# Performance work log

Measured on AMD Instinct MI355X. Metric: run time of the kernel, lower is better.

The kernel has to match this reference:

```python
import jax, jax.numpy as jnp
import numpy as np

B, S, D, H, L = 4, 2048, 512, 8, 128
HD = D // H  # head dim = 64


def setup_inputs() -> dict:
    key = jax.random.key(0)
    ks = jax.random.split(key, 20)
    sc = 0.05
    return {
        "query": jax.random.normal(ks[0], (B, S, D), jnp.float32),
        "key": jax.random.normal(ks[1], (B, S, D), jnp.float32),
        "value": jax.random.normal(ks[2], (B, S, D), jnp.float32),
        "Wq": jax.random.normal(ks[3], (D, D), jnp.float32) * sc,
        "bq": jax.random.normal(ks[4], (D,), jnp.float32) * sc,
        "Wk": jax.random.normal(ks[5], (D, D), jnp.float32) * sc,
        "bk": jax.random.normal(ks[6], (D,), jnp.float32) * sc,
        "Wv": jax.random.normal(ks[7], (D, D), jnp.float32) * sc,
        "bv": jax.random.normal(ks[8], (D,), jnp.float32) * sc,
        "Wo": jax.random.normal(ks[9], (D, D), jnp.float32) * sc,
        "bo": jax.random.normal(ks[10], (D,), jnp.float32) * sc,
        "Wg": jax.random.normal(ks[11], (D, L), jnp.float32) * sc,
        "bg": jax.random.normal(ks[12], (L,), jnp.float32) * sc,
        "Wmq": jax.random.normal(ks[13], (L, D), jnp.float32) * sc,
        "bmq": jax.random.normal(ks[14], (D,), jnp.float32) * sc,
        "Wmk": jax.random.normal(ks[15], (L, D), jnp.float32) * sc,
        "bmk": jax.random.normal(ks[16], (D,), jnp.float32) * sc,
    }


def reference(query, key, value, Wq, bq, Wk, bk, Wv, bv, Wo, bo, Wg, bg, Wmq, bmq, Wmk, bmk):
    # latent-gated modulation of Q and K (computed from query)
    latent = jax.nn.relu(query @ Wg + bg)                 # [B,S,L]
    mod_q = jax.nn.sigmoid(latent @ Wmq + bmq)            # [B,S,D]
    mod_k = jax.nn.sigmoid(latent @ Wmk + bmk)            # [B,S,D]
    q = (query @ Wq + bq) * mod_q
    k = (key @ Wk + bk) * mod_k
    v = value @ Wv + bv
    # split heads: [B,S,D] -> [B,S,H,HD]
    q = q.reshape(B, S, H, HD)
    k = k.reshape(B, S, H, HD)
    v = v.reshape(B, S, H, HD)
    scale = 1.0 / jnp.sqrt(jnp.float32(HD))
    scores = jnp.einsum("bqhd,bkhd->bhqk", q, k) * scale  # [B,H,S,S]
    attn_weights = jax.nn.softmax(scores, axis=-1)
    attn_out = jnp.einsum("bhqk,bkhd->bqhd", attn_weights, v).reshape(B, S, D)
    output = attn_out @ Wo + bo
    return output, attn_weights
```

## Files before the change

### kernel.cpp

```cpp
#include <hip/hip_runtime.h>
#include <hip/hip_bf16.h>

#define BB 4
#define SS 2048
#define DD 512
#define HH 8
#define HDIM 64

typedef __attribute__((ext_vector_type(8))) short bf16x8;
typedef __attribute__((ext_vector_type(4))) float floatx4;
typedef __attribute__((ext_vector_type(8))) unsigned short u16x8;

static __device__ __forceinline__ unsigned short f2bf(float x) {
  __hip_bfloat16 h = __float2bfloat16(x);
  unsigned short u;
  __builtin_memcpy(&u, &h, sizeof(u));
  return u;
}
static __device__ __forceinline__ float bf2f(unsigned short u) {
  union { unsigned int i; float f; } c;
  c.i = ((unsigned int)u) << 16;
  return c.f;
}
static __device__ __forceinline__ void split1(float x, unsigned short& h, unsigned short& l) {
  h = f2bf(x);
  l = f2bf(x - bf2f(h));
}
static __device__ __forceinline__ void gload_lds16(const void* g, void* l) {
  __builtin_amdgcn_global_load_lds((const __attribute__((address_space(1))) void*)g,
                                   (__attribute__((address_space(3))) void*)l, 16, 0, 0);
}

#define SWZ(row, col) ((col) ^ (((row) & 7) * 8))

static __device__ __forceinline__ void stage_tile(unsigned short* dst,
    const unsigned short* src, size_t rstride, int wid, int lane) {
#pragma unroll
  for (int it = 0; it < 2; ++it) {
    const int base = it * 256 + wid * 64;
    const int c = base + lane;
    const int row = c >> 3, uu = c & 7;
    gload_lds16(src + (size_t)row * rstride + ((uu ^ (row & 7)) * 8),
                dst + (size_t)base * 8);
  }
}

__global__ __launch_bounds__(256)
void wsplit_kernel(const float* __restrict__ Wq, const float* __restrict__ Wk,
                   const float* __restrict__ Wv, const float* __restrict__ Wo,
                   const float* __restrict__ Wg, const float* __restrict__ Wmq,
                   const float* __restrict__ Wmk, unsigned short* __restrict__ wsb)
{
  const int bx = blockIdx.x;
  const float* src; unsigned short* dh; unsigned short* dl; int K, N, tile;
  if (bx < 64)       { src = Wq;  dh = wsb + 0;       dl = wsb + 262144;  K = 512; N = 512; tile = bx; }
  else if (bx < 128) { src = Wk;  dh = wsb + 524288;  dl = wsb + 786432;  K = 512; N = 512; tile = bx - 64; }
  else if (bx < 192) { src = Wv;  dh = wsb + 1048576; dl = wsb + 1310720; K = 512; N = 512; tile = bx - 128; }
  else if (bx < 256) { src = Wo;  dh = wsb + 1572864; dl = wsb + 1835008; K = 512; N = 512; tile = bx - 192; }
  else if (bx < 272) { src = Wg;  dh = wsb + 2097152; dl = wsb + 2162688; K = 512; N = 128; tile = bx - 256; }
  else if (bx < 288) { src = Wmq; dh = wsb + 2228224; dl = wsb + 2293760; K = 128; N = 512; tile = bx - 272; }
  else               { src = Wmk; dh = wsb + 2359296; dl = wsb + 2424832; K = 128; N = 512; tile = bx - 288; }
  const int nt = N >> 6;
  const int k0 = (tile / nt) * 64, n0 = (tile % nt) * 64;
  __shared__ float T[64][65];
  const int t = threadIdx.x;
  const int r = t >> 2, c = (t & 3) * 16;
#pragma unroll
  for (int j = 0; j < 16; j += 4)
    *(float4*)&T[r][c + j] = *(const float4*)&src[(size_t)(k0 + r) * N + n0 + c + j];
  __syncthreads();
  u16x8 hv[2], lv[2];
#pragma unroll
  for (int j = 0; j < 16; ++j) {
    unsigned short h, l;
    split1(T[c + j][r], h, l);
    hv[j >> 3][j & 7] = h;
    lv[j >> 3][j & 7] = l;
  }
  const size_t di = (size_t)(n0 + r) * K + k0 + c;
  *(u16x8*)&dh[di]     = hv[0];
  *(u16x8*)&dh[di + 8] = hv[1];
  *(u16x8*)&dl[di]     = lv[0];
  *(u16x8*)&dl[di + 8] = lv[1];
}

template<int BM, int BN>
static __device__ __forceinline__ void gemm_phase(
    const float* __restrict__ A, const unsigned short* __restrict__ WHp,
    const unsigned short* __restrict__ WLp, const int K,
    const int m0, const int n0,
    unsigned short (*Ah)[32], unsigned short (*Al)[32],
    unsigned short (*Bh)[32], unsigned short (*Bl)[32],
    floatx4 (*acc)[BN / 32])
{
  constexpr int HM = BM / 2, HN = BN / 2, FM = BM / 32, FN = BN / 32;
  constexpr int TPR = 256 / BM;
  constexpr int CPT = 32 / TPR;
  constexpr int WCH = BN / 16;
  constexpr int WPW = (2 * WCH) / 4;
  const int t = threadIdx.x;
  const int wid = t >> 6, lane = t & 63, quad = lane >> 4, l16 = lane & 15;
  const int wm = wid >> 1, wn = wid & 1;
  const int arow = t / TPR, acol = (t % TPR) * CPT;
  const int asw = (arow & 3) * 8;

  for (int k0 = 0; k0 < K; k0 += 32) {
    __syncthreads();
#pragma unroll
    for (int cc = 0; cc < WPW; ++cc) {
      const int cid = wid * WPW + cc;
      const int pl = cid / WCH, ch = cid - pl * WCH;
      const int row = ch * 16 + (lane >> 2);
      const int kof = ((lane & 3) ^ ((lane >> 2) & 3)) * 8;
      const unsigned short* g = (pl ? WLp : WHp) + (size_t)(n0 + row) * K + k0 + kof;
      gload_lds16(g, (pl ? Bl : Bh)[ch * 16]);
    }
    {
      const float* ga = A + (size_t)(m0 + arow) * K + k0 + acol;
#pragma unroll
      for (int j = 0; j < CPT; j += 4) {
        float4 f = *(const float4*)(ga + j);
        unsigned short h[4], l[4];
        split1(f.x, h[0], l[0]); split1(f.y, h[1], l[1]);
        split1(f.z, h[2], l[2]); split1(f.w, h[3], l[3]);
        *(ushort4*)&Ah[arow][(acol + j) ^ asw] = make_ushort4(h[0], h[1], h[2], h[3]);
        *(ushort4*)&Al[arow][(acol + j) ^ asw] = make_ushort4(l[0], l[1], l[2], l[3]);
      }
    }
    __syncthreads();
    const int swf = (l16 & 3) * 8;
    bf16x8 fah[FM], fal[FM], fbh[FN], fbl[FN];
#pragma unroll
    for (int mi = 0; mi < FM; ++mi) {
      const int rr = wm * HM + mi * 16 + l16;
      fah[mi] = *(const bf16x8*)&Ah[rr][(quad * 8) ^ swf];
      fal[mi] = *(const bf16x8*)&Al[rr][(quad * 8) ^ swf];
    }
#pragma unroll
    for (int ni = 0; ni < FN; ++ni) {
      const int rr = wn * HN + ni * 16 + l16;
      fbh[ni] = *(const bf16x8*)&Bh[rr][(quad * 8) ^ swf];
      fbl[ni] = *(const bf16x8*)&Bl[rr][(quad * 8) ^ swf];
    }
#pragma unroll
    for (int mi = 0; mi < FM; ++mi)
#pragma unroll
      for (int ni = 0; ni < FN; ++ni) {
        acc[mi][ni] = __builtin_amdgcn_mfma_f32_16x16x32_bf16(fah[mi], fbh[ni], acc[mi][ni], 0, 0, 0);
        acc[mi][ni] = __builtin_amdgcn_mfma_f32_16x16x32_bf16(fal[mi], fbh[ni], acc[mi][ni], 0, 0, 0);
        acc[mi][ni] = __builtin_amdgcn_mfma_f32_16x16x32_bf16(fah[mi], fbl[ni], acc[mi][ni], 0, 0, 0);
      }
  }
}

template<int BM, int BN, int EPI>
__global__ __launch_bounds__(256, 2)
void mgemm_kernel(const float* __restrict__ A, const unsigned short* __restrict__ WH,
                  const unsigned short* __restrict__ WL, const float* __restrict__ bias,
                  const float* __restrict__ modf, const float sc,
                  float* __restrict__ Cf, unsigned short* __restrict__ C16,
                  int K, int N)
{
  constexpr int HM = BM / 2, HN = BN / 2, FM = BM / 32, FN = BN / 32;
  __shared__ alignas(16) unsigned short Ah[BM][32], Al[BM][32], Bh[BN][32], Bl[BN][32];
  const int t = threadIdx.x;
  const int wid = t >> 6, lane = t & 63, quad = lane >> 4, l16 = lane & 15;
  const int wm = wid >> 1, wn = wid & 1;
  const int m0 = blockIdx.y * BM, n0 = blockIdx.x * BN;

  floatx4 acc[FM][FN];
#pragma unroll
  for (int i = 0; i < FM; ++i)
#pragma unroll
    for (int j = 0; j < FN; ++j) {
      floatx4 z = {0.f, 0.f, 0.f, 0.f};
      acc[i][j] = z;
    }

  gemm_phase<BM, BN>(A, WH, WL, K, m0, n0, Ah, Al, Bh, Bl, acc);

#pragma unroll
  for (int ni = 0; ni < FN; ++ni) {
    const int col = n0 + wn * HN + ni * 16 + l16;
    const float b1 = bias[col];
#pragma unroll
    for (int mi = 0; mi < FM; ++mi)
#pragma unroll
      for (int r = 0; r < 4; ++r) {
        const int row = m0 + wm * HM + mi * 16 + quad * 4 + r;
        float v = acc[mi][ni][r] + b1;
        if constexpr (EPI == 0) {
          Cf[(size_t)row * N + col] = v;
        } else if constexpr (EPI == 1) {
          Cf[(size_t)row * N + col] = fmaxf(v, 0.f);
        } else if constexpr (EPI == 2) {
          C16[(size_t)row * N + col] = f2bf(v);
        } else if constexpr (EPI == 4) {
          const float m = modf[(size_t)row * N + col];
          C16[(size_t)row * N + col] = f2bf(v * m * sc);
        } else {
          Cf[(size_t)row * N + col] = 1.f / (1.f + __expf(-v));
        }
      }
  }
}

__global__ __launch_bounds__(256)
void vtrans_kernel(const unsigned short* __restrict__ V16, unsigned short* __restrict__ Vt)
{
  __shared__ unsigned short T[64][72];
  const int x  = blockIdx.x;
  const int st = x & 31;
  const int h  = (x >> 5) & 7;
  const int b  = x >> 8;
  const int t  = threadIdx.x;
  const unsigned short* src = V16 + ((size_t)b * SS + st * 64) * DD + h * HDIM;
  for (int i = t; i < 1024; i += 256) {
    int r = i >> 4, c4 = (i & 15) * 4;
    *(ushort4*)&T[r][c4] = *(const ushort4*)&src[(size_t)r * DD + c4];
  }
  __syncthreads();
  unsigned short* dst = Vt + ((size_t)(b * HH + h) * HDIM) * SS + st * 64;
  for (int i = t; i < 1024; i += 256) {
    int hd = i >> 4, s4 = (i & 15) * 4;
    ushort4 u = make_ushort4(T[s4 + 0][hd], T[s4 + 1][hd], T[s4 + 2][hd], T[s4 + 3][hd]);
    *(ushort4*)&dst[(size_t)hd * SS + s4] = u;
  }
}

__global__ __launch_bounds__(256, 3)
void attn_kernel(const unsigned short* __restrict__ Q16,
                 const unsigned short* __restrict__ K16,
                 const unsigned short* __restrict__ Vt,
                 float* __restrict__ AW, float* __restrict__ AO)
{
  __shared__ alignas(16) unsigned short Qs[64][64];
  __shared__ alignas(16) unsigned short Ks[2][64][64];
  __shared__ alignas(16) unsigned short Vs[2][64][64];
  __shared__ alignas(16) unsigned short Ps[4][16][64];

  const int t    = threadIdx.x;
  const int wid  = t >> 6;
  const int lane = t & 63;
  const int quad = lane >> 4;
  const int l16  = lane & 15;
  const int x  = blockIdx.x;
  const int j  = x >> 3;
  const int g  = ((j >> 5) << 3) | (x & 7);
  const int qb = j & 31;
  const int b  = g >> 3;
  const int h  = g & 7;
  const int q0 = qb * 64;

  const unsigned short* Qg = Q16 + ((size_t)b * SS + q0) * DD + h * HDIM;
  const unsigned short* Kg = K16 + (size_t)b * SS * DD + h * HDIM;
  const unsigned short* Vg = Vt + ((size_t)(b * HH + h) * HDIM) * SS;

  stage_tile(&Qs[0][0], Qg, DD, wid, lane);
  stage_tile(&Ks[0][0][0], Kg, DD, wid, lane);
  __syncthreads();

  const bf16x8 a0 = *(const bf16x8*)&Qs[wid * 16 + l16][SWZ(l16, quad * 8)];
  const bf16x8 a1 = *(const bf16x8*)&Qs[wid * 16 + l16][SWZ(l16, 32 + quad * 8)];

  float lsum[4] = {0.f, 0.f, 0.f, 0.f};
  for (int kt = 0; kt < SS / 64; ++kt) {
    const int cur = kt & 1;
    if (kt < 31)
      stage_tile(&Ks[cur ^ 1][0][0], Kg + (size_t)(kt + 1) * 64 * DD, DD, wid, lane);
#pragma unroll
    for (int kst = 0; kst < 4; ++kst) {
      bf16x8 bb0 = *(const bf16x8*)&Ks[cur][kst * 16 + l16][SWZ(l16, quad * 8)];
      bf16x8 bb1 = *(const bf16x8*)&Ks[cur][kst * 16 + l16][SWZ(l16, 32 + quad * 8)];
      floatx4 cc = {0.f, 0.f, 0.f, 0.f};
      cc = __builtin_amdgcn_mfma_f32_16x16x32_bf16(a0, bb0, cc, 0, 0, 0);
      cc = __builtin_amdgcn_mfma_f32_16x16x32_bf16(a1, bb1, cc, 0, 0, 0);
#pragma unroll
      for (int r = 0; r < 4; ++r) lsum[r] += __expf(cc[r]);
    }
    __syncthreads();
  }
#pragma unroll
  for (int r = 0; r < 4; ++r) {
    float v = lsum[r];
    v += __shfl_xor(v, 1, 64); v += __shfl_xor(v, 2, 64);
    v += __shfl_xor(v, 4, 64); v += __shfl_xor(v, 8, 64);
    lsum[r] = 1.f / v;
  }

  floatx4 o[4];
#pragma unroll
  for (int n = 0; n < 4; ++n) { floatx4 z = {0.f, 0.f, 0.f, 0.f}; o[n] = z; }

  const size_t awb = ((size_t)(b * HH + h) * SS + q0 + wid * 16) * SS;

  stage_tile(&Ks[0][0][0], Kg, DD, wid, lane);
  stage_tile(&Vs[0][0][0], Vg, SS, wid, lane);
  __syncthreads();
  for (int kt = 0; kt < SS / 64; ++kt) {
    const int cur = kt & 1;
    if (kt < 31) {
      stage_tile(&Ks[cur ^ 1][0][0], Kg + (size_t)(kt + 1) * 64 * DD, DD, wid, lane);
      stage_tile(&Vs[cur ^ 1][0][0], Vg + (size_t)(kt + 1) * 64, SS, wid, lane);
    }
#pragma unroll
    for (int kst = 0; kst < 4; ++kst) {
      bf16x8 bb0 = *(const bf16x8*)&Ks[cur][kst * 16 + l16][SWZ(l16, quad * 8)];
      bf16x8 bb1 = *(const bf16x8*)&Ks[cur][kst * 16 + l16][SWZ(l16, 32 + quad * 8)];
      floatx4 cc = {0.f, 0.f, 0.f, 0.f};
      cc = __builtin_amdgcn_mfma_f32_16x16x32_bf16(a0, bb0, cc, 0, 0, 0);
      cc = __builtin_amdgcn_mfma_f32_16x16x32_bf16(a1, bb1, cc, 0, 0, 0);
#pragma unroll
      for (int r = 0; r < 4; ++r) {
        const float wv = __expf(cc[r]) * lsum[r];
        AW[awb + (size_t)(quad * 4 + r) * SS + kt * 64 + kst * 16 + l16] = wv;
        Ps[wid][quad * 4 + r][SWZ(quad * 4 + r, kst * 16 + l16)] = f2bf(wv);
      }
    }
#pragma unroll
    for (int c2 = 0; c2 < 2; ++c2) {
      bf16x8 ap = *(const bf16x8*)&Ps[wid][l16][SWZ(l16, c2 * 32 + quad * 8)];
#pragma unroll
      for (int n = 0; n < 4; ++n) {
        bf16x8 bv = *(const bf16x8*)&Vs[cur][n * 16 + l16][SWZ(l16, c2 * 32 + quad * 8)];
        o[n] = __builtin_amdgcn_mfma_f32_16x16x32_bf16(ap, bv, o[n], 0, 0, 0);
      }
    }
    __syncthreads();
  }
  float* AOg = AO + ((size_t)b * SS + q0 + wid * 16) * DD + h * HDIM;
#pragma unroll
  for (int n = 0; n < 4; ++n)
#pragma unroll
    for (int r = 0; r < 4; ++r)
      AOg[(size_t)(quad * 4 + r) * DD + n * 16 + l16] = o[n][r];
}

extern "C" void kernel_launch(void* const* d_in, const int* in_sizes, int n_in,
                              void* d_out, int out_size, void* d_ws, size_t ws_size,
                              hipStream_t stream) {
  (void)in_sizes; (void)n_in; (void)out_size; (void)ws_size;
  const float* query = (const float*)d_in[0];
  const float* key_i = (const float*)d_in[1];
  const float* value = (const float*)d_in[2];
  const float* Wq  = (const float*)d_in[3];
  const float* bq  = (const float*)d_in[4];
  const float* Wk  = (const float*)d_in[5];
  const float* bk  = (const float*)d_in[6];
  const float* Wv  = (const float*)d_in[7];
  const float* bv  = (const float*)d_in[8];
  const float* Wo  = (const float*)d_in[9];
  const float* bo  = (const float*)d_in[10];
  const float* Wg  = (const float*)d_in[11];
  const float* bg  = (const float*)d_in[12];
  const float* Wmq = (const float*)d_in[13];
  const float* bmq = (const float*)d_in[14];
  const float* Wmk = (const float*)d_in[15];
  const float* bmk = (const float*)d_in[16];

  float* out = (float*)d_out;
  float* AW  = out + (size_t)BB * SS * DD;

  char* ws = (char*)d_ws;
  unsigned short* ws16 = (unsigned short*)ws;
  unsigned short* q16 = (unsigned short*)(ws + (5u  << 20));
  unsigned short* k16 = (unsigned short*)(ws + (13u << 20));
  unsigned short* vt  = (unsigned short*)(ws + (21u << 20));
  float*          lat = (float*)(ws + (29u << 20));
  float*          X   = (float*)(ws + (33u << 20));
  unsigned short* v16 = (unsigned short*)(ws + (33u << 20));
  float*          ao  = (float*)(ws + (33u << 20));

  const size_t W_WQH = 0,       W_WQL = 262144;
  const size_t W_WKH = 524288,  W_WKL = 786432;
  const size_t W_WVH = 1048576, W_WVL = 1310720;
  const size_t W_WOH = 1572864, W_WOL = 1835008;
  const size_t W_WGH = 2097152, W_WGL = 2162688;
  const size_t W_WMQH = 2228224, W_WMQL = 2293760;
  const size_t W_WMKH = 2359296, W_WMKL = 2424832;

  dim3 blk(256);
  wsplit_kernel<<<dim3(304), blk, 0, stream>>>(Wq, Wk, Wv, Wo, Wg, Wmq, Wmk, ws16);
  mgemm_kernel<64, 64, 1><<<dim3(2, 128), blk, 0, stream>>>(
      query, ws16 + W_WGH, ws16 + W_WGL, bg, nullptr, 1.f, lat, nullptr, 512, 128);
  mgemm_kernel<64, 64, 5><<<dim3(8, 128), blk, 0, stream>>>(
      lat, ws16 + W_WMQH, ws16 + W_WMQL, bmq, nullptr, 1.f, X, nullptr, 128, 512);
  mgemm_kernel<128, 64, 4><<<dim3(8, 64), blk, 0, stream>>>(
      query, ws16 + W_WQH, ws16 + W_WQL, bq, X, 0.125f, nullptr, q16, 512, 512);
  mgemm_kernel<64, 64, 5><<<dim3(8, 128), blk, 0, stream>>>(
      lat, ws16 + W_WMKH, ws16 + W_WMKL, bmk, nullptr, 1.f, X, nullptr, 128, 512);
  mgemm_kernel<128, 64, 4><<<dim3(8, 64), blk, 0, stream>>>(
      key_i, ws16 + W_WKH, ws16 + W_WKL, bk, X, 1.f, nullptr, k16, 512, 512);
  mgemm_kernel<128, 64, 2><<<dim3(8, 64), blk, 0, stream>>>(
      value, ws16 + W_WVH, ws16 + W_WVL, bv, nullptr, 1.f, nullptr, v16, 512, 512);
  vtrans_kernel<<<dim3(1024), blk, 0, stream>>>(v16, vt);
  attn_kernel<<<dim3(1024), blk, 0, stream>>>(q16, k16, vt, AW, ao);
  mgemm_kernel<128, 64, 0><<<dim3(8, 64), blk, 0, stream>>>(
      ao, ws16 + W_WOH, ws16 + W_WOL, bo, nullptr, 1.f, out, nullptr, 512, 512);
}
```

Before: 865.9 us.

## Split attention row-sum pass into separate split-K kernel with 4x more blocks

The first pass that computes softmax denominators moves out of the attention kernel into its own kernel. That kernel splits the key dimension into four chunks across 4096 blocks and writes partial sums to workspace. The P·V kernel then reads and adds the four partials, and its Q fragments now load straight from global memory instead of through shared memory. The aim is more parallelism in the denominator pass and lower per-block latency in the main kernel. The cost is an extra launch, a partial-sum buffer, and dropping the occupancy hint of 3 blocks per SM.

```diff
diff --git a/kernel.cpp b/kernel.cpp
--- a/kernel.cpp
+++ b/kernel.cpp
@@ -228,45 +228,36 @@
   }
 }
 
-__global__ __launch_bounds__(256, 3)
-void attn_kernel(const unsigned short* __restrict__ Q16,
-                 const unsigned short* __restrict__ K16,
-                 const unsigned short* __restrict__ Vt,
-                 float* __restrict__ AW, float* __restrict__ AO)
-{
-  __shared__ alignas(16) unsigned short Qs[64][64];
+__global__ __launch_bounds__(256)
+void attn_lsum_kernel(const unsigned short* __restrict__ Q16,
+                      const unsigned short* __restrict__ K16,
+                      float* __restrict__ lsum4)
+{
   __shared__ alignas(16) unsigned short Ks[2][64][64];
-  __shared__ alignas(16) unsigned short Vs[2][64][64];
-  __shared__ alignas(16) unsigned short Ps[4][16][64];
-
-  const int t    = threadIdx.x;
-  const int wid  = t >> 6;
-  const int lane = t & 63;
-  const int quad = lane >> 4;
-  const int l16  = lane & 15;
-  const int x  = blockIdx.x;
-  const int j  = x >> 3;
-  const int g  = ((j >> 5) << 3) | (x & 7);
+  const int t = threadIdx.x, wid = t >> 6, lane = t & 63;
+  const int quad = lane >> 4, l16 = lane & 15;
+  const int x = blockIdx.x;
+  const int c = x >> 10;
+  const int y = x & 1023;
+  const int j = y >> 3;
+  const int g = ((j >> 5) << 3) | (y & 7);
   const int qb = j & 31;
-  const int b  = g >> 3;
-  const int h  = g & 7;
+  const int b = g >> 3, h = g & 7;
   const int q0 = qb * 64;
 
   const unsigned short* Qg = Q16 + ((size_t)b * SS + q0) * DD + h * HDIM;
-  const unsigned short* Kg = K16 + (size_t)b * SS * DD + h * HDIM;
-  const unsigned short* Vg = Vt + ((size_t)(b * HH + h) * HDIM) * SS;
-
-  stage_tile(&Qs[0][0], Qg, DD, wid, lane);
+  const unsigned short* Kg = K16 + (size_t)b * SS * DD + h * HDIM + (size_t)c * 512 * DD;
+
+  const bf16x8 a0 = *(const bf16x8*)&Qg[(size_t)(wid * 16 + l16) * DD + quad * 8];
+  const bf16x8 a1 = *(const bf16x8*)&Qg[(size_t)(wid * 16 + l16) * DD + 32 + quad * 8];
+
   stage_tile(&Ks[0][0][0], Kg, DD, wid, lane);
   __syncthreads();
 
-  const bf16x8 a0 = *(const bf16x8*)&Qs[wid * 16 + l16][SWZ(l16, quad * 8)];
-  const bf16x8 a1 = *(const bf16x8*)&Qs[wid * 16 + l16][SWZ(l16, 32 + quad * 8)];
-
   float lsum[4] = {0.f, 0.f, 0.f, 0.f};
-  for (int kt = 0; kt < SS / 64; ++kt) {
+  for (int kt = 0; kt < 8; ++kt) {
     const int cur = kt & 1;
-    if (kt < 31)
+    if (kt < 7)
       stage_tile(&Ks[cur ^ 1][0][0], Kg + (size_t)(kt + 1) * 64 * DD, DD, wid, lane);
 #pragma unroll
     for (int kst = 0; kst < 4; ++kst) {
@@ -285,18 +276,55 @@
     float v = lsum[r];
     v += __shfl_xor(v, 1, 64); v += __shfl_xor(v, 2, 64);
     v += __shfl_xor(v, 4, 64); v += __shfl_xor(v, 8, 64);
-    lsum[r] = 1.f / v;
-  }
-
-  floatx4 o[4];
-#pragma unroll
-  for (int n = 0; n < 4; ++n) { floatx4 z = {0.f, 0.f, 0.f, 0.f}; o[n] = z; }
-
-  const size_t awb = ((size_t)(b * HH + h) * SS + q0 + wid * 16) * SS;
+    if (l16 == 0)
+      lsum4[((size_t)g * SS + q0 + wid * 16 + quad * 4 + r) * 4 + c] = v;
+  }
+}
+
+__global__ __launch_bounds__(256)
+void attn_pv_kernel(const unsigned short* __restrict__ Q16,
+                    const unsigned short* __restrict__ K16,
+                    const unsigned short* __restrict__ Vt,
+                    const float* __restrict__ lsum4,
+                    float* __restrict__ AW, float* __restrict__ AO)
+{
+  __shared__ alignas(16) unsigned short Ks[2][64][64];
+  __shared__ alignas(16) unsigned short Vs[2][64][64];
+  __shared__ alignas(16) unsigned short Ps[4][16][64];
+
+  const int t = threadIdx.x, wid = t >> 6, lane = t & 63;
+  const int quad = lane >> 4, l16 = lane & 15;
+  const int x = blockIdx.x;
+  const int j = x >> 3;
+  const int g = ((j >> 5) << 3) | (x & 7);
+  const int qb = j & 31;
+  const int b = g >> 3, h = g & 7;
+  const int q0 = qb * 64;
+
+  const unsigned short* Qg = Q16 + ((size_t)b * SS + q0) * DD + h * HDIM;
+  const unsigned short* Kg = K16 + (size_t)b * SS * DD + h * HDIM;
+  const unsigned short* Vg = Vt + ((size_t)(b * HH + h) * HDIM) * SS;
+
+  const bf16x8 a0 = *(const bf16x8*)&Qg[(size_t)(wid * 16 + l16) * DD + quad * 8];
+  const bf16x8 a1 = *(const bf16x8*)&Qg[(size_t)(wid * 16 + l16) * DD + 32 + quad * 8];
+
+  float inv_l[4];
+#pragma unroll
+  for (int r = 0; r < 4; ++r) {
+    float4 lv = *(const float4*)&lsum4[((size_t)g * SS + q0 + wid * 16 + quad * 4 + r) * 4];
+    inv_l[r] = 1.f / (lv.x + lv.y + lv.z + lv.w);
+  }
 
   stage_tile(&Ks[0][0][0], Kg, DD, wid, lane);
   stage_tile(&Vs[0][0][0], Vg, SS, wid, lane);
   __syncthreads();
+
+  floatx4 o[4];
+#pragma unroll
+  for (int n = 0; n < 4; ++n) { floatx4 z = {0.f, 0.f, 0.f, 0.f}; o[n] = z; }
+
+  const size_t awb = ((size_t)g * SS + q0 + wid * 16) * SS;
+
   for (int kt = 0; kt < SS / 64; ++kt) {
     const int cur = kt & 1;
     if (kt < 31) {
@@ -312,7 +340,7 @@
       cc = __builtin_amdgcn_mfma_f32_16x16x32_bf16(a1, bb1, cc, 0, 0, 0);
 #pragma unroll
       for (int r = 0; r < 4; ++r) {
-        const float wv = __expf(cc[r]) * lsum[r];
+        const float wv = __expf(cc[r]) * inv_l[r];
         AW[awb + (size_t)(quad * 4 + r) * SS + kt * 64 + kst * 16 + l16] = wv;
         Ps[wid][quad * 4 + r][SWZ(quad * 4 + r, kst * 16 + l16)] = f2bf(wv);
       }
@@ -370,6 +398,7 @@
   float*          X   = (float*)(ws + (33u << 20));
   unsigned short* v16 = (unsigned short*)(ws + (33u << 20));
   float*          ao  = (float*)(ws + (33u << 20));
+  float*          lsum4 = (float*)(ws + (49u << 20));
 
   const size_t W_WQH = 0,       W_WQL = 262144;
   const size_t W_WKH = 524288,  W_WKL = 786432;
@@ -391,10 +420,11 @@
       lat, ws16 + W_WMKH, ws16 + W_WMKL, bmk, nullptr, 1.f, X, nullptr, 128, 512);
   mgemm_kernel<128, 64, 4><<<dim3(8, 64), blk, 0, stream>>>(
       key_i, ws16 + W_WKH, ws16 + W_WKL, bk, X, 1.f, nullptr, k16, 512, 512);
+  attn_lsum_kernel<<<dim3(4096), blk, 0, stream>>>(q16, k16, lsum4);
   mgemm_kernel<128, 64, 2><<<dim3(8, 64), blk, 0, stream>>>(
       value, ws16 + W_WVH, ws16 + W_WVL, bv, nullptr, 1.f, nullptr, v16, 512, 512);
   vtrans_kernel<<<dim3(1024), blk, 0, stream>>>(v16, vt);
-  attn_kernel<<<dim3(1024), blk, 0, stream>>>(q16, k16, vt, AW, ao);
+  attn_pv_kernel<<<dim3(1024), blk, 0, stream>>>(q16, k16, vt, lsum4, AW, ao);
   mgemm_kernel<128, 64, 0><<<dim3(8, 64), blk, 0, stream>>>(
       ao, ws16 + W_WOH, ws16 + W_WOL, bo, nullptr, 1.f, out, nullptr, 512, 512);
 }
```

New measurement: 854.0 us. No clear change (-1.4%).
